# Kernel optimization log

Measured on AMD Instinct MI355X. Metric: run time of the kernel, lower is better.

Reference implementation:

```python
import jax, jax.numpy as jnp
import numpy as np

N_NODES = 50000
N_EDGES = 800000
IN_C, HID_C, OUT_C = 128, 128, 64
BN_EPS = 1e-5


def setup_inputs() -> dict:
    key = jax.random.key(0)
    ks = jax.random.split(key, 12)
    def lin(k, fan_in, fan_out):
        bound = 1.0 / np.sqrt(fan_in)
        kw, kb = jax.random.split(k)
        W = jax.random.uniform(kw, (fan_in, fan_out), jnp.float32, -bound, bound)
        b = jax.random.uniform(kb, (fan_out,), jnp.float32, -bound, bound)
        return W, b
    x = jax.random.normal(ks[0], (N_NODES, IN_C), jnp.float32)
    edge_index = jax.random.randint(ks[1], (2, N_EDGES), 0, N_NODES, jnp.int32)
    w1a, b1a = lin(ks[2], IN_C, HID_C)
    w1b, b1b = lin(ks[3], HID_C, HID_C)
    w2a, b2a = lin(ks[4], HID_C, OUT_C)
    w2b, b2b = lin(ks[5], OUT_C, OUT_C)
    return {
        "x": x, "edge_index": edge_index,
        "w1a": w1a, "b1a": b1a, "g1": jnp.ones((HID_C,)), "be1": jnp.zeros((HID_C,)),
        "w1b": w1b, "b1b": b1b,
        "w2a": w2a, "b2a": b2a, "g2": jnp.ones((OUT_C,)), "be2": jnp.zeros((OUT_C,)),
        "w2b": w2b, "b2b": b2b,
    }


def _batchnorm(h, gamma, beta):
    # training-style BN over node dim, biased variance (torch BatchNorm1d)
    mean = jnp.mean(h, axis=0)
    var = jnp.mean(jnp.square(h - mean), axis=0)
    return (h - mean) * jax.lax.rsqrt(var + BN_EPS) * gamma + beta


def _gin_layer(x, src, dst, n_nodes, w_a, b_a, gamma, beta, w_b, b_b):
    # GINConv with eps=0: MLP(x + sum_{j->i} x_j)
    agg = jax.ops.segment_sum(x[src], dst, num_segments=n_nodes)  # [N, C]
    h = x + agg
    h = h @ w_a + b_a
    h = jax.nn.relu(_batchnorm(h, gamma, beta))
    return h @ w_b + b_b


def reference(x, edge_index, w1a, b1a, g1, be1, w1b, b1b, w2a, b2a, g2, be2, w2b, b2b):
    src, dst = edge_index[0], edge_index[1]
    n = x.shape[0]
    h = _gin_layer(x, src, dst, n, w1a, b1a, g1, be1, w1b, b1b)
    h = jax.nn.relu(h)  # dropout p=0.0 -> identity
    h = _gin_layer(h, src, dst, n, w2a, b2a, g2, be2, w2b, b2b)
    return jax.nn.log_softmax(h, axis=-1)
```

## Files before the change

### kernel.cpp

```cpp
#include <hip/hip_runtime.h>


typedef unsigned short u16;
typedef unsigned int u32;
typedef __attribute__((ext_vector_type(8))) short short8;
typedef __attribute__((ext_vector_type(4))) short short4v;
typedef __attribute__((ext_vector_type(4))) float f32x4;

#define DEV_INLINE __device__ __forceinline__

DEV_INLINE void atomAddF(float* p, float v) { unsafeAtomicAdd(p, v); }

DEV_INLINE u16 f2bf(float f) {
    unsigned u = __float_as_uint(f);
    u += 0x7fffu + ((u >> 16) & 1u);
    return (u16)(u >> 16);
}
DEV_INLINE float bf2f(u16 h) { return __uint_as_float(((unsigned)h) << 16); }

__global__ __launch_bounds__(256) void wprep4_k(
    const float* __restrict__ w1a, const float* __restrict__ w1b,
    const float* __restrict__ w2a, const float* __restrict__ w2b,
    short* __restrict__ o1a, short* __restrict__ o1b,
    short* __restrict__ o2a, short* __restrict__ o2b)
{
    int b = blockIdx.x;
    const float* W; short* wf; int K, NOUT;
    if (b < 8)       { W = w1a; wf = o1a; K = 128; NOUT = 128; }
    else if (b < 16) { W = w1b; wf = o1b; K = 128; NOUT = 128; b -= 8; }
    else if (b < 20) { W = w2a; wf = o2a; K = 128; NOUT = 64;  b -= 16; }
    else             { W = w2b; wf = o2b; K = 64;  NOUT = 64;  b -= 20; }
    const int u = b * 256 + threadIdx.x;
    const int units = (NOUT / 16) * (K / 32) * 64;
    if (u >= units) return;
    const int per_ct = (K / 32) * 64;
    const int ct = u / per_ct;
    const int rem = u % per_ct;
    const int kc = rem >> 6;
    const int l = rem & 63;
    const int col = ct * 16 + (l & 15);
    const int k0 = kc * 32 + (l >> 4) * 8;
    short8 pk;
#pragma unroll
    for (int j = 0; j < 8; j++)
        pk[j] = (short)f2bf(W[(size_t)(k0 + j) * NOUT + col]);
    *(short8*)&wf[(size_t)u * 8] = pk;
}

__global__ __launch_bounds__(256) void mgemm1_k(
    const float* __restrict__ x, const short* __restrict__ wf,
    u16* __restrict__ p1, int M)
{
    constexpr int KD = 128, NC = 128, KC = 4, KQ = 32;
    __shared__ short Asl[64 * KD];
    const int t = threadIdx.x;
    const int l = t & 63;
    const int w = t >> 6;

    short8 B[2][KC];
#pragma unroll
    for (int c = 0; c < 2; c++)
#pragma unroll
        for (int kc = 0; kc < KC; kc++)
            B[c][kc] = *(const short8*)&wf[(((w * 2 + c) * KC + kc) * 64 + l) * 8];

    {
        const int r = t >> 2;
        const int q = t & 3;
        const int grow = blockIdx.x * 64 + r;
        const int rt = r >> 4;
        u16 hv[KQ];
        if (grow < M) {
            const float* ap = x + (size_t)grow * KD + q * KQ;
#pragma unroll
            for (int i = 0; i < KQ / 4; i++) {
                const float4 v = ((const float4*)ap)[i];
                hv[i * 4 + 0] = f2bf(v.x); hv[i * 4 + 1] = f2bf(v.y);
                hv[i * 4 + 2] = f2bf(v.z); hv[i * 4 + 3] = f2bf(v.w);
            }
        } else {
#pragma unroll
            for (int i = 0; i < KQ; i++) hv[i] = 0;
        }
#pragma unroll
        for (int gg = 0; gg < KQ / 8; gg++) {
            const int k0 = q * KQ + gg * 8;
            const int kc = k0 >> 5;
            const int lane = (r & 15) + ((k0 >> 3) & 3) * 16;
            *(short8*)&Asl[((rt * KC + kc) * 64 + lane) * 8] = *(short8*)&hv[gg * 8];
        }
    }
    __syncthreads();

    f32x4 acc[4][2];
#pragma unroll
    for (int rt = 0; rt < 4; rt++)
#pragma unroll
        for (int c = 0; c < 2; c++) acc[rt][c] = (f32x4){0.f, 0.f, 0.f, 0.f};

#pragma unroll
    for (int kc = 0; kc < KC; kc++)
#pragma unroll
        for (int rt = 0; rt < 4; rt++) {
            const short8 x0 = *(const short8*)&Asl[((rt * KC + kc) * 64 + l) * 8];
            acc[rt][0] = __builtin_amdgcn_mfma_f32_16x16x32_bf16(B[0][kc], x0, acc[rt][0], 0, 0, 0);
            acc[rt][1] = __builtin_amdgcn_mfma_f32_16x16x32_bf16(B[1][kc], x0, acc[rt][1], 0, 0, 0);
        }

    const int cbase = (l >> 4) * 4;
#pragma unroll
    for (int rt = 0; rt < 4; rt++) {
        const int grow = blockIdx.x * 64 + rt * 16 + (l & 15);
        if (grow < M) {
#pragma unroll
            for (int c = 0; c < 2; c++) {
                short4v o16;
#pragma unroll
                for (int j = 0; j < 4; j++) o16[j] = (short)f2bf(acc[rt][c][j]);
                *(short4v*)&p1[(size_t)grow * NC + (w * 2 + c) * 16 + cbase] = o16;
            }
        }
    }
}

__global__ __launch_bounds__(256) void mgemm23_k(
    const u16* __restrict__ s1, const short* __restrict__ w1bf,
    const short* __restrict__ w2af,
    const float* __restrict__ sum, const float* __restrict__ sumsq,
    const float* __restrict__ g, const float* __restrict__ be, float invN,
    const float* __restrict__ b1b, u16* __restrict__ p2, int M)
{
    constexpr int KD = 128, NC = 128, NO = 64, KC = 4, KQ = 32;
    __shared__ short Asl[64 * KD];
    __shared__ float scb[KD];
    __shared__ float shb[KD];

    const int t = threadIdx.x;
    const int l = t & 63;
    const int w = t >> 6;

    short8 B1[2][KC];
    short8 B2[KC];
#pragma unroll
    for (int c = 0; c < 2; c++)
#pragma unroll
        for (int kc = 0; kc < KC; kc++)
            B1[c][kc] = *(const short8*)&w1bf[(((w * 2 + c) * KC + kc) * 64 + l) * 8];
#pragma unroll
    for (int kc = 0; kc < KC; kc++)
        B2[kc] = *(const short8*)&w2af[((w * KC + kc) * 64 + l) * 8];

    if (t < KD) {
        const float m = sum[t] * invN;
        const float v = sumsq[t] * invN - m * m;
        const float r = rsqrtf(v + 1e-5f);
        const float s = g[t] * r;
        scb[t] = s;
        shb[t] = be[t] - m * s;
    }
    __syncthreads();

    {
        const int r = t >> 2;
        const int q = t & 3;
        const int grow = blockIdx.x * 64 + r;
        const int rt = r >> 4;
        u16 hv[KQ];
        if (grow < M) {
            const u16* ap = s1 + (size_t)grow * KD + q * KQ;
#pragma unroll
            for (int i = 0; i < KQ / 8; i++)
                *(short8*)&hv[i * 8] = ((const short8*)ap)[i];
#pragma unroll
            for (int i = 0; i < KQ; i++) {
                const int k = q * KQ + i;
                hv[i] = f2bf(fmaxf(0.f, bf2f(hv[i]) * scb[k] + shb[k]));
            }
        } else {
#pragma unroll
            for (int i = 0; i < KQ; i++) hv[i] = 0;
        }
#pragma unroll
        for (int gg = 0; gg < KQ / 8; gg++) {
            const int k0 = q * KQ + gg * 8;
            const int kc = k0 >> 5;
            const int lane = (r & 15) + ((k0 >> 3) & 3) * 16;
            *(short8*)&Asl[((rt * KC + kc) * 64 + lane) * 8] = *(short8*)&hv[gg * 8];
        }
    }
    __syncthreads();

    f32x4 acc[4][2];
#pragma unroll
    for (int rt = 0; rt < 4; rt++)
#pragma unroll
        for (int c = 0; c < 2; c++) acc[rt][c] = (f32x4){0.f, 0.f, 0.f, 0.f};
#pragma unroll
    for (int kc = 0; kc < KC; kc++)
#pragma unroll
        for (int rt = 0; rt < 4; rt++) {
            const short8 x0 = *(const short8*)&Asl[((rt * KC + kc) * 64 + l) * 8];
            acc[rt][0] = __builtin_amdgcn_mfma_f32_16x16x32_bf16(B1[0][kc], x0, acc[rt][0], 0, 0, 0);
            acc[rt][1] = __builtin_amdgcn_mfma_f32_16x16x32_bf16(B1[1][kc], x0, acc[rt][1], 0, 0, 0);
        }
    __syncthreads();

    {
        const int cb4 = l >> 4;
#pragma unroll
        for (int rt = 0; rt < 4; rt++) {
            const int row = rt * 16 + (l & 15);
            const int sw = (row & 7) << 1;
#pragma unroll
            for (int c = 0; c < 2; c++) {
                const int ct = w * 2 + c;
                const float4 bv = *(const float4*)&b1b[ct * 16 + cb4 * 4];
                short4v o16;
                o16[0] = (short)f2bf(fmaxf(acc[rt][c][0] + bv.x, 0.f));
                o16[1] = (short)f2bf(fmaxf(acc[rt][c][1] + bv.y, 0.f));
                o16[2] = (short)f2bf(fmaxf(acc[rt][c][2] + bv.z, 0.f));
                o16[3] = (short)f2bf(fmaxf(acc[rt][c][3] + bv.w, 0.f));
                const int gsw = (ct * 4 + cb4) ^ sw;
                *(short4v*)&Asl[row * 128 + gsw * 4] = o16;
            }
        }
    }
    __syncthreads();

    f32x4 acc2[4];
#pragma unroll
    for (int rt = 0; rt < 4; rt++) acc2[rt] = (f32x4){0.f, 0.f, 0.f, 0.f};
#pragma unroll
    for (int kc = 0; kc < KC; kc++)
#pragma unroll
        for (int rt = 0; rt < 4; rt++) {
            const int row = rt * 16 + (l & 15);
            const int G = kc * 8 + (l >> 4) * 2;
            const int Gs = G ^ ((row & 7) << 1);
            const short8 x0 = *(const short8*)&Asl[row * 128 + Gs * 4];
            acc2[rt] = __builtin_amdgcn_mfma_f32_16x16x32_bf16(B2[kc], x0, acc2[rt], 0, 0, 0);
        }

    {
        const int cbase = (l >> 4) * 4;
#pragma unroll
        for (int rt = 0; rt < 4; rt++) {
            const int grow = blockIdx.x * 64 + rt * 16 + (l & 15);
            if (grow < M) {
                short4v o16;
#pragma unroll
                for (int j = 0; j < 4; j++) o16[j] = (short)f2bf(acc2[rt][j]);
                *(short4v*)&p2[(size_t)grow * NO + w * 16 + cbase] = o16;
            }
        }
    }
}

__global__ __launch_bounds__(256) void mgemm4_k(
    const u16* __restrict__ s2, const short* __restrict__ Wf,
    const float* __restrict__ sum, const float* __restrict__ sumsq,
    const float* __restrict__ g, const float* __restrict__ be, float invN,
    const float* __restrict__ bias, float* __restrict__ outp, int M)
{
    constexpr int KD = 64, NC = 64, KC = 2, CT = 4, KQ = 16;
    __shared__ short Asl[64 * KD];
    __shared__ short Bsl[NC * KD];
    __shared__ float scb[KD];
    __shared__ float shb[KD];

    const int t = threadIdx.x;
    const int l = t & 63;
    const int w = t >> 6;

    if (t < KD) {
        const float m = sum[t] * invN;
        const float v = sumsq[t] * invN - m * m;
        const float r = rsqrtf(v + 1e-5f);
        const float s = g[t] * r;
        scb[t] = s;
        shb[t] = be[t] - m * s;
    }
    __syncthreads();

    {
        const float4* src = (const float4*)Wf;
        float4* dst = (float4*)Bsl;
#pragma unroll
        for (int u = t; u < NC * KD / 8; u += 256) dst[u] = src[u];
    }
    {
        const int r = t >> 2;
        const int q = t & 3;
        const int grow = blockIdx.x * 64 + r;
        const int rt = r >> 4;
        u16 hv[KQ];
        if (grow < M) {
            const u16* ap = s2 + (size_t)grow * KD + q * KQ;
#pragma unroll
            for (int i = 0; i < KQ / 8; i++)
                *(short8*)&hv[i * 8] = ((const short8*)ap)[i];
#pragma unroll
            for (int i = 0; i < KQ; i++) {
                const int k = q * KQ + i;
                hv[i] = f2bf(fmaxf(0.f, bf2f(hv[i]) * scb[k] + shb[k]));
            }
        } else {
#pragma unroll
            for (int i = 0; i < KQ; i++) hv[i] = 0;
        }
#pragma unroll
        for (int gg = 0; gg < KQ / 8; gg++) {
            const int k0 = q * KQ + gg * 8;
            const int kc = k0 >> 5;
            const int lane = (r & 15) + ((k0 >> 3) & 3) * 16;
            *(short8*)&Asl[((rt * KC + kc) * 64 + lane) * 8] = *(short8*)&hv[gg * 8];
        }
    }
    __syncthreads();

    f32x4 acc[CT];
#pragma unroll
    for (int c = 0; c < CT; c++) acc[c] = (f32x4){0.f, 0.f, 0.f, 0.f};
#pragma unroll
    for (int kc = 0; kc < KC; kc++) {
        const short8 x0 = *(const short8*)&Asl[((w * KC + kc) * 64 + l) * 8];
#pragma unroll
        for (int ct = 0; ct < CT; ct++) {
            const short8 wb = *(const short8*)&Bsl[((ct * KC + kc) * 64 + l) * 8];
            acc[ct] = __builtin_amdgcn_mfma_f32_16x16x32_bf16(wb, x0, acc[ct], 0, 0, 0);
        }
    }

    const int cbase = (l >> 4) * 4;
    const int grow = blockIdx.x * 64 + w * 16 + (l & 15);
    float v[CT * 4];
#pragma unroll
    for (int ct = 0; ct < CT; ct++) {
        const float4 bv = *(const float4*)&bias[ct * 16 + cbase];
        v[ct * 4 + 0] = acc[ct][0] + bv.x;
        v[ct * 4 + 1] = acc[ct][1] + bv.y;
        v[ct * 4 + 2] = acc[ct][2] + bv.z;
        v[ct * 4 + 3] = acc[ct][3] + bv.w;
    }
    float m = v[0];
#pragma unroll
    for (int j = 1; j < CT * 4; j++) m = fmaxf(m, v[j]);
    m = fmaxf(m, __shfl_xor(m, 16));
    m = fmaxf(m, __shfl_xor(m, 32));
    float s = 0.f;
#pragma unroll
    for (int j = 0; j < CT * 4; j++) s += __expf(v[j] - m);
    s += __shfl_xor(s, 16);
    s += __shfl_xor(s, 32);
    const float lg = m + __logf(s);
    if (grow < M) {
#pragma unroll
        for (int ct = 0; ct < CT; ct++) {
            f32x4 o;
#pragma unroll
            for (int j = 0; j < 4; j++) o[j] = v[ct * 4 + j] - lg;
            *(f32x4*)&outp[(size_t)grow * NC + ct * 16 + cbase] = o;
        }
    }
}

__global__ __launch_bounds__(256) void hist_k(const int* __restrict__ ei,
                                              int* __restrict__ cnt,
                                              int* __restrict__ agg, int E)
{
    const int gid = blockIdx.x * blockDim.x + threadIdx.x;
    if (gid < 256) agg[gid] = 0;
    const int stride = gridDim.x * blockDim.x;
    for (int e = gid; e < E; e += stride) atomicAdd(&cnt[ei[E + e]], 1);
}

__global__ __launch_bounds__(256) void scan1_k(const int* __restrict__ cnt,
                                               int* __restrict__ agg,
                                               int* __restrict__ off,
                                               int* __restrict__ cursor,
                                               int N, int E)
{
    __shared__ int part[256];
    __shared__ int redu[256];
    const int t = threadIdx.x;
    const int b = blockIdx.x;
    const int i = b * 256 + t;
    const int v = (i < N) ? cnt[i] : 0;
    part[t] = v;
    __syncthreads();
    for (int d = 1; d < 256; d <<= 1) {
        const int u = (t >= d) ? part[t - d] : 0;
        __syncthreads();
        part[t] += u;
        __syncthreads();
    }
    if (t == 0)
        __hip_atomic_store(&agg[b], part[255] | (1 << 30), __ATOMIC_RELEASE,
                           __HIP_MEMORY_SCOPE_AGENT);
    int loc = 0;
    for (int pb = t; pb < b; pb += 256) {
        int a;
        do {
            a = __hip_atomic_load(&agg[pb], __ATOMIC_ACQUIRE,
                                  __HIP_MEMORY_SCOPE_AGENT);
        } while (!(a & (1 << 30)));
        loc += a & ((1 << 30) - 1);
    }
    redu[t] = loc;
    __syncthreads();
    for (int s = 128; s; s >>= 1) {
        if (t < s) redu[t] += redu[t + s];
        __syncthreads();
    }
    const int base = redu[0];
    if (i < N) {
        const int o = base + part[t] - v;
        off[i] = o;
        cursor[i] = o;
    }
    if (b == 0 && t == 0) off[N] = E;
}

__global__ __launch_bounds__(256) void fill_k(const int* __restrict__ ei,
                                              int* __restrict__ cursor,
                                              int* __restrict__ srcs, int E)
{
    const int gid = blockIdx.x * blockDim.x + threadIdx.x;
    const int stride = gridDim.x * blockDim.x;
    for (int e = gid; e < E; e += stride) {
        const int s = ei[e];
        const int d = ei[E + e];
        const int pos = atomicAdd(&cursor[d], 1);
        srcs[pos] = s;
    }
}

template <int C>
__global__ __launch_bounds__(256) void segsum_bf(
    const u16* __restrict__ p, const int* __restrict__ off,
    const int* __restrict__ srcs, u16* __restrict__ out,
    float* __restrict__ sum, float* __restrict__ sumsq, int N)
{
    constexpr int BLKN = 8;
    constexpr int VPL = C / 64;
    __shared__ float red[4][64][2 * VPL];

    const int wv = threadIdx.x >> 6;
    const int l  = threadIdx.x & 63;
    const int base = blockIdx.x * 4 * BLKN;

    float ss[VPL], qq[VPL];
#pragma unroll
    for (int v = 0; v < VPL; v++) { ss[v] = 0.f; qq[v] = 0.f; }

    for (int i = 0; i < BLKN; i++) {
        const int n = base + i * 4 + wv;
        if (n < N) {
            const int lo = __builtin_amdgcn_readfirstlane(off[n]);
            const int hi = __builtin_amdgcn_readfirstlane(off[n + 1]);
            float acc[VPL];
            if constexpr (VPL == 2) {
                const u32 u = *(const u32*)&p[(size_t)n * C + 2 * l];
                acc[0] = bf2f((u16)u);
                acc[1] = bf2f((u16)(u >> 16));
            } else {
                acc[0] = bf2f(p[(size_t)n * C + l]);
            }
            const int cnt = hi - lo;
            if (cnt > 0) {
                const int last = hi - 1;
                int idx[8];
#pragma unroll
                for (int j = 0; j < 8; j++) idx[j] = srcs[min(lo + j, last)];
                for (int e = lo; e < hi; e += 8) {
                    int nx[8];
#pragma unroll
                    for (int j = 0; j < 8; j++)
                        nx[j] = srcs[min(e + 8 + j, last)];
#pragma unroll
                    for (int j = 0; j < 8; j++) {
                        const bool live = (e + j) < hi;
                        if constexpr (VPL == 2) {
                            const u32 u = *(const u32*)&p[(size_t)idx[j] * C + 2 * l];
                            const float v0 = bf2f((u16)u);
                            const float v1 = bf2f((u16)(u >> 16));
                            acc[0] += live ? v0 : 0.f;
                            acc[1] += live ? v1 : 0.f;
                        } else {
                            const float v = bf2f(p[(size_t)idx[j] * C + l]);
                            acc[0] += live ? v : 0.f;
                        }
                    }
#pragma unroll
                    for (int j = 0; j < 8; j++) idx[j] = nx[j];
                }
            }
            if constexpr (VPL == 2) {
                const u16 r0 = f2bf(acc[0]);
                const u16 r1 = f2bf(acc[1]);
                *(u32*)&out[(size_t)n * C + 2 * l] = (u32)r0 | ((u32)r1 << 16);
                const float f0 = bf2f(r0), f1 = bf2f(r1);
                ss[0] += f0; qq[0] += f0 * f0;
                ss[1] += f1; qq[1] += f1 * f1;
            } else {
                const u16 r = f2bf(acc[0]);
                out[(size_t)n * C + l] = r;
                const float f = bf2f(r);
                ss[0] += f; qq[0] += f * f;
            }
        }
    }

#pragma unroll
    for (int v = 0; v < VPL; v++) {
        red[wv][l][2 * v] = ss[v];
        red[wv][l][2 * v + 1] = qq[v];
    }
    __syncthreads();
    if (wv == 0) {
#pragma unroll
        for (int v = 0; v < VPL; v++) {
            float a = 0.f, b = 0.f;
#pragma unroll
            for (int w2 = 0; w2 < 4; w2++) {
                a += red[w2][l][2 * v];
                b += red[w2][l][2 * v + 1];
            }
            const int ch = (VPL == 2) ? (2 * l + v) : l;
            atomAddF(&sum[ch], a);
            atomAddF(&sumsq[ch], b);
        }
    }
}

extern "C" void kernel_launch(void* const* d_in, const int* in_sizes, int n_in,
                              void* d_out, int out_size, void* d_ws, size_t ws_size,
                              hipStream_t stream)
{
    const float* x   = (const float*)d_in[0];
    const int*   ei  = (const int*)d_in[1];
    const float* w1a = (const float*)d_in[2];
    const float* g1  = (const float*)d_in[4];
    const float* be1 = (const float*)d_in[5];
    const float* w1b = (const float*)d_in[6];
    const float* b1b = (const float*)d_in[7];
    const float* w2a = (const float*)d_in[8];
    const float* g2  = (const float*)d_in[10];
    const float* be2 = (const float*)d_in[11];
    const float* w2b = (const float*)d_in[12];
    const float* b2b = (const float*)d_in[13];
    float* out = (float*)d_out;

    const int N = in_sizes[0] / 128;
    const int E = in_sizes[1] / 2;

    u16* buf1 = (u16*)d_ws;
    u16* buf2 = buf1 + (size_t)N * 128;
    float* stats = (float*)(buf2 + (size_t)N * 128);
    float* sum1 = stats,       *sq1 = stats + 128;
    float* sum2 = stats + 256, *sq2 = stats + 320;
    int* cnt    = (int*)(stats + 1024);
    int* off    = cnt + N;
    int* cursor = off + N + 1;
    int* srcs   = cursor + N;
    int* agg    = srcs + E;
    int* bpre   = agg + 256;
    short* w1af = (short*)(bpre + 256);
    short* w1bf = w1af + 128 * 128;
    short* w2af = w1bf + 128 * 128;
    short* w2bf = w2af + 128 * 64;
    u16* p1 = buf1;
    u16* s1 = buf2;
    u16* p2 = buf1;
    u16* s2 = buf2;

    hipMemsetAsync(stats, 0, 1024 * sizeof(float) + (size_t)N * sizeof(int), stream);

    const int G1 = (N + 255) / 256;
    const int gb = (N + 63) / 64;
    const int gs = (N + 31) / 32;
    const float invN = 1.f / N;

    hist_k<<<1024, 256, 0, stream>>>(ei, cnt, agg, E);
    scan1_k<<<G1, 256, 0, stream>>>(cnt, agg, off, cursor, N, E);
    fill_k<<<1024, 256, 0, stream>>>(ei, cursor, srcs, E);

    wprep4_k<<<22, 256, 0, stream>>>(w1a, w1b, w2a, w2b, w1af, w1bf, w2af, w2bf);

    mgemm1_k<<<gb, 256, 0, stream>>>(x, w1af, p1, N);
    segsum_bf<128><<<gs, 256, 0, stream>>>(p1, off, srcs, s1, sum1, sq1, N);

    mgemm23_k<<<gb, 256, 0, stream>>>(s1, w1bf, w2af, sum1, sq1, g1, be1,
                                      invN, b1b, p2, N);

    segsum_bf<64><<<gs, 256, 0, stream>>>(p2, off, srcs, s2, sum2, sq2, N);
    mgemm4_k<<<gb, 256, 0, stream>>>(s2, w2bf, sum2, sq2, g2, be2, invN, b2b,
                                     out, N);
}
```

Baseline: 290.6 us.

## Merge first GEMM, weight prep, and degree histogram into one heterogeneous launch

Combines mgemm1, the weight-preparation kernel and the edge histogram into a single kernel whose blocks pick their role by block index. The first GEMM now converts w1a to bf16 fragments inline from fp32 global memory instead of reading a prepacked buffer. This removes two launches and the serialization between independent stages, letting the GEMM and histogram atomics overlap. The cost is redundant per-block strided weight conversion and a mixed-role grid that may load-balance unevenly.

```diff
diff --git a/kernel.cpp b/kernel.cpp
--- a/kernel.cpp
+++ b/kernel.cpp
@@ -18,360 +18,127 @@
 }
 DEV_INLINE float bf2f(u16 h) { return __uint_as_float(((unsigned)h) << 16); }
 
-__global__ __launch_bounds__(256) void wprep4_k(
-    const float* __restrict__ w1a, const float* __restrict__ w1b,
-    const float* __restrict__ w2a, const float* __restrict__ w2b,
-    short* __restrict__ o1a, short* __restrict__ o1b,
-    short* __restrict__ o2a, short* __restrict__ o2b)
+__global__ __launch_bounds__(256) void fat1_k(
+    const float* __restrict__ x, const float* __restrict__ w1a,
+    u16* __restrict__ p1, int M, int gb,
+    const int* __restrict__ ei, int* __restrict__ cnt,
+    int* __restrict__ agg, int E,
+    const float* __restrict__ w1b, const float* __restrict__ w2a,
+    const float* __restrict__ w2b,
+    short* __restrict__ o1b, short* __restrict__ o2a,
+    short* __restrict__ o2b)
 {
-    int b = blockIdx.x;
-    const float* W; short* wf; int K, NOUT;
-    if (b < 8)       { W = w1a; wf = o1a; K = 128; NOUT = 128; }
-    else if (b < 16) { W = w1b; wf = o1b; K = 128; NOUT = 128; b -= 8; }
-    else if (b < 20) { W = w2a; wf = o2a; K = 128; NOUT = 64;  b -= 16; }
-    else             { W = w2b; wf = o2b; K = 64;  NOUT = 64;  b -= 20; }
-    const int u = b * 256 + threadIdx.x;
-    const int units = (NOUT / 16) * (K / 32) * 64;
-    if (u >= units) return;
-    const int per_ct = (K / 32) * 64;
-    const int ct = u / per_ct;
-    const int rem = u % per_ct;
-    const int kc = rem >> 6;
-    const int l = rem & 63;
-    const int col = ct * 16 + (l & 15);
-    const int k0 = kc * 32 + (l >> 4) * 8;
-    short8 pk;
-#pragma unroll
-    for (int j = 0; j < 8; j++)
-        pk[j] = (short)f2bf(W[(size_t)(k0 + j) * NOUT + col]);
-    *(short8*)&wf[(size_t)u * 8] = pk;
-}
-
-__global__ __launch_bounds__(256) void mgemm1_k(
-    const float* __restrict__ x, const short* __restrict__ wf,
-    u16* __restrict__ p1, int M)
-{
-    constexpr int KD = 128, NC = 128, KC = 4, KQ = 32;
-    __shared__ short Asl[64 * KD];
+    __shared__ short Asl[64 * 128];
+    const int bid = blockIdx.x;
     const int t = threadIdx.x;
-    const int l = t & 63;
-    const int w = t >> 6;
-
-    short8 B[2][KC];
-#pragma unroll
-    for (int c = 0; c < 2; c++)
+
+    if (bid < gb) {
+        constexpr int KD = 128, NC = 128, KC = 4, KQ = 32;
+        const int l = t & 63;
+        const int w = t >> 6;
+
+        short8 B[2][KC];
+#pragma unroll
+        for (int c = 0; c < 2; c++) {
+            const int col = (w * 2 + c) * 16 + (l & 15);
+#pragma unroll
+            for (int kc = 0; kc < KC; kc++) {
+                const int k0 = kc * 32 + (l >> 4) * 8;
+                short8 b;
+#pragma unroll
+                for (int j = 0; j < 8; j++)
+                    b[j] = (short)f2bf(w1a[(size_t)(k0 + j) * NC + col]);
+                B[c][kc] = b;
+            }
+        }
+
+        {
+            const int r = t >> 2;
+            const int q = t & 3;
+            const int grow = bid * 64 + r;
+            const int rt = r >> 4;
+            u16 hv[KQ];
+            if (grow < M) {
+                const float* ap = x + (size_t)grow * KD + q * KQ;
+#pragma unroll
+                for (int i = 0; i < KQ / 4; i++) {
+                    const float4 v = ((const float4*)ap)[i];
+                    hv[i * 4 + 0] = f2bf(v.x); hv[i * 4 + 1] = f2bf(v.y);
+                    hv[i * 4 + 2] = f2bf(v.z); hv[i * 4 + 3] = f2bf(v.w);
+                }
+            } else {
+#pragma unroll
+                for (int i = 0; i < KQ; i++) hv[i] = 0;
+            }
+#pragma unroll
+            for (int gg = 0; gg < KQ / 8; gg++) {
+                const int k0 = q * KQ + gg * 8;
+                const int kc = k0 >> 5;
+                const int lane = (r & 15) + ((k0 >> 3) & 3) * 16;
+                *(short8*)&Asl[((rt * KC + kc) * 64 + lane) * 8] =
+                    *(short8*)&hv[gg * 8];
+            }
+        }
+        __syncthreads();
+
+        f32x4 acc[4][2];
+#pragma unroll
+        for (int rt = 0; rt < 4; rt++)
+#pragma unroll
+            for (int c = 0; c < 2; c++) acc[rt][c] = (f32x4){0.f, 0.f, 0.f, 0.f};
+
 #pragma unroll
         for (int kc = 0; kc < KC; kc++)
-            B[c][kc] = *(const short8*)&wf[(((w * 2 + c) * KC + kc) * 64 + l) * 8];
-
-    {
-        const int r = t >> 2;
-        const int q = t & 3;
-        const int grow = blockIdx.x * 64 + r;
-        const int rt = r >> 4;
-        u16 hv[KQ];
-        if (grow < M) {
-            const float* ap = x + (size_t)grow * KD + q * KQ;
-#pragma unroll
-            for (int i = 0; i < KQ / 4; i++) {
-                const float4 v = ((const float4*)ap)[i];
-                hv[i * 4 + 0] = f2bf(v.x); hv[i * 4 + 1] = f2bf(v.y);
-                hv[i * 4 + 2] = f2bf(v.z); hv[i * 4 + 3] = f2bf(v.w);
-            }
-        } else {
-#pragma unroll
-            for (int i = 0; i < KQ; i++) hv[i] = 0;
-        }
-#pragma unroll
-        for (int gg = 0; gg < KQ / 8; gg++) {
-            const int k0 = q * KQ + gg * 8;
-            const int kc = k0 >> 5;
-            const int lane = (r & 15) + ((k0 >> 3) & 3) * 16;
-            *(short8*)&Asl[((rt * KC + kc) * 64 + lane) * 8] = *(short8*)&hv[gg * 8];
-        }
-    }
-    __syncthreads();
-
-    f32x4 acc[4][2];
-#pragma unroll
-    for (int rt = 0; rt < 4; rt++)
-#pragma unroll
-        for (int c = 0; c < 2; c++) acc[rt][c] = (f32x4){0.f, 0.f, 0.f, 0.f};
-
-#pragma unroll
-    for (int kc = 0; kc < KC; kc++)
+#pragma unroll
+            for (int rt = 0; rt < 4; rt++) {
+                const short8 x0 = *(const short8*)&Asl[((rt * KC + kc) * 64 + l) * 8];
+                acc[rt][0] = __builtin_amdgcn_mfma_f32_16x16x32_bf16(B[0][kc], x0, acc[rt][0], 0, 0, 0);
+                acc[rt][1] = __builtin_amdgcn_mfma_f32_16x16x32_bf16(B[1][kc], x0, acc[rt][1], 0, 0, 0);
+            }
+
+        const int cbase = (l >> 4) * 4;
 #pragma unroll
         for (int rt = 0; rt < 4; rt++) {
-            const short8 x0 = *(const short8*)&Asl[((rt * KC + kc) * 64 + l) * 8];
-            acc[rt][0] = __builtin_amdgcn_mfma_f32_16x16x32_bf16(B[0][kc], x0, acc[rt][0], 0, 0, 0);
-            acc[rt][1] = __builtin_amdgcn_mfma_f32_16x16x32_bf16(B[1][kc], x0, acc[rt][1], 0, 0, 0);
-        }
-
-    const int cbase = (l >> 4) * 4;
-#pragma unroll
-    for (int rt = 0; rt < 4; rt++) {
-        const int grow = blockIdx.x * 64 + rt * 16 + (l & 15);
-        if (grow < M) {
-#pragma unroll
-            for (int c = 0; c < 2; c++) {
-                short4v o16;
-#pragma unroll
-                for (int j = 0; j < 4; j++) o16[j] = (short)f2bf(acc[rt][c][j]);
-                *(short4v*)&p1[(size_t)grow * NC + (w * 2 + c) * 16 + cbase] = o16;
-            }
-        }
-    }
-}
-
-__global__ __launch_bounds__(256) void mgemm23_k(
-    const u16* __restrict__ s1, const short* __restrict__ w1bf,
-    const short* __restrict__ w2af,
-    const float* __restrict__ sum, const float* __restrict__ sumsq,
-    const float* __restrict__ g, const float* __restrict__ be, float invN,
-    const float* __restrict__ b1b, u16* __restrict__ p2, int M)
-{
-    constexpr int KD = 128, NC = 128, NO = 64, KC = 4, KQ = 32;
-    __shared__ short Asl[64 * KD];
-    __shared__ float scb[KD];
-    __shared__ float shb[KD];
-
-    const int t = threadIdx.x;
-    const int l = t & 63;
-    const int w = t >> 6;
-
-    short8 B1[2][KC];
-    short8 B2[KC];
-#pragma unroll
-    for (int c = 0; c < 2; c++)
-#pragma unroll
-        for (int kc = 0; kc < KC; kc++)
-            B1[c][kc] = *(const short8*)&w1bf[(((w * 2 + c) * KC + kc) * 64 + l) * 8];
-#pragma unroll
-    for (int kc = 0; kc < KC; kc++)
-        B2[kc] = *(const short8*)&w2af[((w * KC + kc) * 64 + l) * 8];
-
-    if (t < KD) {
-        const float m = sum[t] * invN;
-        const float v = sumsq[t] * invN - m * m;
-        const float r = rsqrtf(v + 1e-5f);
-        const float s = g[t] * r;
-        scb[t] = s;
-        shb[t] = be[t] - m * s;
-    }
-    __syncthreads();
-
-    {
-        const int r = t >> 2;
-        const int q = t & 3;
-        const int grow = blockIdx.x * 64 + r;
-        const int rt = r >> 4;
-        u16 hv[KQ];
-        if (grow < M) {
-            const u16* ap = s1 + (size_t)grow * KD + q * KQ;
-#pragma unroll
-            for (int i = 0; i < KQ / 8; i++)
-                *(short8*)&hv[i * 8] = ((const short8*)ap)[i];
-#pragma unroll
-            for (int i = 0; i < KQ; i++) {
-                const int k = q * KQ + i;
-                hv[i] = f2bf(fmaxf(0.f, bf2f(hv[i]) * scb[k] + shb[k]));
-            }
-        } else {
-#pragma unroll
-            for (int i = 0; i < KQ; i++) hv[i] = 0;
-        }
-#pragma unroll
-        for (int gg = 0; gg < KQ / 8; gg++) {
-            const int k0 = q * KQ + gg * 8;
-            const int kc = k0 >> 5;
-            const int lane = (r & 15) + ((k0 >> 3) & 3) * 16;
-            *(short8*)&Asl[((rt * KC + kc) * 64 + lane) * 8] = *(short8*)&hv[gg * 8];
-        }
-    }
-    __syncthreads();
-
-    f32x4 acc[4][2];
-#pragma unroll
-    for (int rt = 0; rt < 4; rt++)
-#pragma unroll
-        for (int c = 0; c < 2; c++) acc[rt][c] = (f32x4){0.f, 0.f, 0.f, 0.f};
-#pragma unroll
-    for (int kc = 0; kc < KC; kc++)
-#pragma unroll
-        for (int rt = 0; rt < 4; rt++) {
-            const short8 x0 = *(const short8*)&Asl[((rt * KC + kc) * 64 + l) * 8];
-            acc[rt][0] = __builtin_amdgcn_mfma_f32_16x16x32_bf16(B1[0][kc], x0, acc[rt][0], 0, 0, 0);
-            acc[rt][1] = __builtin_amdgcn_mfma_f32_16x16x32_bf16(B1[1][kc], x0, acc[rt][1], 0, 0, 0);
-        }
-    __syncthreads();
-
-    {
-        const int cb4 = l >> 4;
-#pragma unroll
-        for (int rt = 0; rt < 4; rt++) {
-            const int row = rt * 16 + (l & 15);
-            const int sw = (row & 7) << 1;
-#pragma unroll
-            for (int c = 0; c < 2; c++) {
-                const int ct = w * 2 + c;
-                const float4 bv = *(const float4*)&b1b[ct * 16 + cb4 * 4];
-                short4v o16;
-                o16[0] = (short)f2bf(fmaxf(acc[rt][c][0] + bv.x, 0.f));
-                o16[1] = (short)f2bf(fmaxf(acc[rt][c][1] + bv.y, 0.f));
-                o16[2] = (short)f2bf(fmaxf(acc[rt][c][2] + bv.z, 0.f));
-                o16[3] = (short)f2bf(fmaxf(acc[rt][c][3] + bv.w, 0.f));
-                const int gsw = (ct * 4 + cb4) ^ sw;
-                *(short4v*)&Asl[row * 128 + gsw * 4] = o16;
-            }
-        }
-    }
-    __syncthreads();
-
-    f32x4 acc2[4];
-#pragma unroll
-    for (int rt = 0; rt < 4; rt++) acc2[rt] = (f32x4){0.f, 0.f, 0.f, 0.f};
-#pragma unroll
-    for (int kc = 0; kc < KC; kc++)
-#pragma unroll
-        for (int rt = 0; rt < 4; rt++) {
-            const int row = rt * 16 + (l & 15);
-            const int G = kc * 8 + (l >> 4) * 2;
-            const int Gs = G ^ ((row & 7) << 1);
-            const short8 x0 = *(const short8*)&Asl[row * 128 + Gs * 4];
-            acc2[rt] = __builtin_amdgcn_mfma_f32_16x16x32_bf16(B2[kc], x0, acc2[rt], 0, 0, 0);
-        }
-
-    {
-        const int cbase = (l >> 4) * 4;
-#pragma unroll
-        for (int rt = 0; rt < 4; rt++) {
-            const int grow = blockIdx.x * 64 + rt * 16 + (l & 15);
+            const int grow = bid * 64 + rt * 16 + (l & 15);
             if (grow < M) {
-                short4v o16;
-#pragma unroll
-                for (int j = 0; j < 4; j++) o16[j] = (short)f2bf(acc2[rt][j]);
-                *(short4v*)&p2[(size_t)grow * NO + w * 16 + cbase] = o16;
-            }
-        }
-    }
-}
-
-__global__ __launch_bounds__(256) void mgemm4_k(
-    const u16* __restrict__ s2, const short* __restrict__ Wf,
-    const float* __restrict__ sum, const float* __restrict__ sumsq,
-    const float* __restrict__ g, const float* __restrict__ be, float invN,
-    const float* __restrict__ bias, float* __restrict__ outp, int M)
-{
-    constexpr int KD = 64, NC = 64, KC = 2, CT = 4, KQ = 16;
-    __shared__ short Asl[64 * KD];
-    __shared__ short Bsl[NC * KD];
-    __shared__ float scb[KD];
-    __shared__ float shb[KD];
-
-    const int t = threadIdx.x;
-    const int l = t & 63;
-    const int w = t >> 6;
-
-    if (t < KD) {
-        const float m = sum[t] * invN;
-        const float v = sumsq[t] * invN - m * m;
-        const float r = rsqrtf(v + 1e-5f);
-        const float s = g[t] * r;
-        scb[t] = s;
-        shb[t] = be[t] - m * s;
-    }
-    __syncthreads();
-
-    {
-        const float4* src = (const float4*)Wf;
-        float4* dst = (float4*)Bsl;
-#pragma unroll
-        for (int u = t; u < NC * KD / 8; u += 256) dst[u] = src[u];
-    }
-    {
-        const int r = t >> 2;
-        const int q = t & 3;
-        const int grow = blockIdx.x * 64 + r;
-        const int rt = r >> 4;
-        u16 hv[KQ];
-        if (grow < M) {
-            const u16* ap = s2 + (size_t)grow * KD + q * KQ;
-#pragma unroll
-            for (int i = 0; i < KQ / 8; i++)
-                *(short8*)&hv[i * 8] = ((const short8*)ap)[i];
-#pragma unroll
-            for (int i = 0; i < KQ; i++) {
-                const int k = q * KQ + i;
-                hv[i] = f2bf(fmaxf(0.f, bf2f(hv[i]) * scb[k] + shb[k]));
-            }
-        } else {
-#pragma unroll
-            for (int i = 0; i < KQ; i++) hv[i] = 0;
-        }
-#pragma unroll
-        for (int gg = 0; gg < KQ / 8; gg++) {
-            const int k0 = q * KQ + gg * 8;
-            const int kc = k0 >> 5;
-            const int lane = (r & 15) + ((k0 >> 3) & 3) * 16;
-            *(short8*)&Asl[((rt * KC + kc) * 64 + lane) * 8] = *(short8*)&hv[gg * 8];
-        }
-    }
-    __syncthreads();
-
-    f32x4 acc[CT];
-#pragma unroll
-    for (int c = 0; c < CT; c++) acc[c] = (f32x4){0.f, 0.f, 0.f, 0.f};
-#pragma unroll
-    for (int kc = 0; kc < KC; kc++) {
-        const short8 x0 = *(const short8*)&Asl[((w * KC + kc) * 64 + l) * 8];
-#pragma unroll
-        for (int ct = 0; ct < CT; ct++) {
-            const short8 wb = *(const short8*)&Bsl[((ct * KC + kc) * 64 + l) * 8];
-            acc[ct] = __builtin_amdgcn_mfma_f32_16x16x32_bf16(wb, x0, acc[ct], 0, 0, 0);
-        }
-    }
-
-    const int cbase = (l >> 4) * 4;
-    const int grow = blockIdx.x * 64 + w * 16 + (l & 15);
-    float v[CT * 4];
-#pragma unroll
-    for (int ct = 0; ct < CT; ct++) {
-        const float4 bv = *(const float4*)&bias[ct * 16 + cbase];
-        v[ct * 4 + 0] = acc[ct][0] + bv.x;
-        v[ct * 4 + 1] = acc[ct][1] + bv.y;
-        v[ct * 4 + 2] = acc[ct][2] + bv.z;
-        v[ct * 4 + 3] = acc[ct][3] + bv.w;
-    }
-    float m = v[0];
-#pragma unroll
-    for (int j = 1; j < CT * 4; j++) m = fmaxf(m, v[j]);
-    m = fmaxf(m, __shfl_xor(m, 16));
-    m = fmaxf(m, __shfl_xor(m, 32));
-    float s = 0.f;
-#pragma unroll
-    for (int j = 0; j < CT * 4; j++) s += __expf(v[j] - m);
-    s += __shfl_xor(s, 16);
-    s += __shfl_xor(s, 32);
-    const float lg = m + __logf(s);
-    if (grow < M) {
-#pragma unroll
-        for (int ct = 0; ct < CT; ct++) {
-            f32x4 o;
-#pragma unroll
-            for (int j = 0; j < 4; j++) o[j] = v[ct * 4 + j] - lg;
-            *(f32x4*)&outp[(size_t)grow * NC + ct * 16 + cbase] = o;
-        }
-    }
-}
-
-__global__ __launch_bounds__(256) void hist_k(const int* __restrict__ ei,
-                                              int* __restrict__ cnt,
-                                              int* __restrict__ agg, int E)
-{
-    const int gid = blockIdx.x * blockDim.x + threadIdx.x;
-    if (gid < 256) agg[gid] = 0;
-    const int stride = gridDim.x * blockDim.x;
-    for (int e = gid; e < E; e += stride) atomicAdd(&cnt[ei[E + e]], 1);
+#pragma unroll
+                for (int c = 0; c < 2; c++) {
+                    short4v o16;
+#pragma unroll
+                    for (int j = 0; j < 4; j++) o16[j] = (short)f2bf(acc[rt][c][j]);
+                    *(short4v*)&p1[(size_t)grow * NC + (w * 2 + c) * 16 + cbase] = o16;
+                }
+            }
+        }
+    } else if (bid < gb + 14) {
+        int b = bid - gb;
+        const float* W; short* wf; int K, NOUT;
+        if (b < 8)       { W = w1b; wf = o1b; K = 128; NOUT = 128; }
+        else if (b < 12) { W = w2a; wf = o2a; K = 128; NOUT = 64;  b -= 8; }
+        else             { W = w2b; wf = o2b; K = 64;  NOUT = 64;  b -= 12; }
+        const int u = b * 256 + t;
+        const int units = (NOUT / 16) * (K / 32) * 64;
+        if (u < units) {
+            const int per_ct = (K / 32) * 64;
+            const int ct = u / per_ct;
+            const int rem = u % per_ct;
+            const int kc = rem >> 6;
+            const int l = rem & 63;
+            const int col = ct * 16 + (l & 15);
+            const int k0 = kc * 32 + (l >> 4) * 8;
+            short8 pk;
+#pragma unroll
+            for (int j = 0; j < 8; j++)
+                pk[j] = (short)f2bf(W[(size_t)(k0 + j) * NOUT + col]);
+            *(short8*)&wf[(size_t)u * 8] = pk;
+        }
+    } else {
+        const int hb = bid - gb - 14;
+        const int gid = hb * 256 + t;
+        if (gid < 256) agg[gid] = 0;
+        const int stride = (gridDim.x - gb - 14) * 256;
+        for (int e = gid; e < E; e += stride) atomicAdd(&cnt[ei[E + e]], 1);
+    }
 }
 
 __global__ __launch_bounds__(256) void scan1_k(const int* __restrict__ cnt,
@@ -432,6 +199,247 @@
         const int d = ei[E + e];
         const int pos = atomicAdd(&cursor[d], 1);
         srcs[pos] = s;
+    }
+}
+
+__global__ __launch_bounds__(256) void mgemm23_k(
+    const u16* __restrict__ s1, const short* __restrict__ w1bf,
+    const short* __restrict__ w2af,
+    const float* __restrict__ sum, const float* __restrict__ sumsq,
+    const float* __restrict__ g, const float* __restrict__ be, float invN,
+    const float* __restrict__ b1b, u16* __restrict__ p2, int M)
+{
+    constexpr int KD = 128, NO = 64, KC = 4, KQ = 32;
+    __shared__ short Asl[64 * KD];
+    __shared__ float scb[KD];
+    __shared__ float shb[KD];
+
+    const int t = threadIdx.x;
+    const int l = t & 63;
+    const int w = t >> 6;
+
+    short8 B1[2][KC];
+    short8 B2[KC];
+#pragma unroll
+    for (int c = 0; c < 2; c++)
+#pragma unroll
+        for (int kc = 0; kc < KC; kc++)
+            B1[c][kc] = *(const short8*)&w1bf[(((w * 2 + c) * KC + kc) * 64 + l) * 8];
+#pragma unroll
+    for (int kc = 0; kc < KC; kc++)
+        B2[kc] = *(const short8*)&w2af[((w * KC + kc) * 64 + l) * 8];
+
+    if (t < KD) {
+        const float m = sum[t] * invN;
+        const float v = sumsq[t] * invN - m * m;
+        const float r = rsqrtf(v + 1e-5f);
+        const float s = g[t] * r;
+        scb[t] = s;
+        shb[t] = be[t] - m * s;
+    }
+    __syncthreads();
+
+    {
+        const int r = t >> 2;
+        const int q = t & 3;
+        const int grow = blockIdx.x * 64 + r;
+        const int rt = r >> 4;
+        u16 hv[KQ];
+        if (grow < M) {
+            const u16* ap = s1 + (size_t)grow * KD + q * KQ;
+#pragma unroll
+            for (int i = 0; i < KQ / 8; i++)
+                *(short8*)&hv[i * 8] = ((const short8*)ap)[i];
+#pragma unroll
+            for (int i = 0; i < KQ; i++) {
+                const int k = q * KQ + i;
+                hv[i] = f2bf(fmaxf(0.f, bf2f(hv[i]) * scb[k] + shb[k]));
+            }
+        } else {
+#pragma unroll
+            for (int i = 0; i < KQ; i++) hv[i] = 0;
+        }
+#pragma unroll
+        for (int gg = 0; gg < KQ / 8; gg++) {
+            const int k0 = q * KQ + gg * 8;
+            const int kc = k0 >> 5;
+            const int lane = (r & 15) + ((k0 >> 3) & 3) * 16;
+            *(short8*)&Asl[((rt * KC + kc) * 64 + lane) * 8] = *(short8*)&hv[gg * 8];
+        }
+    }
+    __syncthreads();
+
+    f32x4 acc[4][2];
+#pragma unroll
+    for (int rt = 0; rt < 4; rt++)
+#pragma unroll
+        for (int c = 0; c < 2; c++) acc[rt][c] = (f32x4){0.f, 0.f, 0.f, 0.f};
+#pragma unroll
+    for (int kc = 0; kc < KC; kc++)
+#pragma unroll
+        for (int rt = 0; rt < 4; rt++) {
+            const short8 x0 = *(const short8*)&Asl[((rt * KC + kc) * 64 + l) * 8];
+            acc[rt][0] = __builtin_amdgcn_mfma_f32_16x16x32_bf16(B1[0][kc], x0, acc[rt][0], 0, 0, 0);
+            acc[rt][1] = __builtin_amdgcn_mfma_f32_16x16x32_bf16(B1[1][kc], x0, acc[rt][1], 0, 0, 0);
+        }
+    __syncthreads();
+
+    {
+        const int cb4 = l >> 4;
+#pragma unroll
+        for (int rt = 0; rt < 4; rt++) {
+            const int row = rt * 16 + (l & 15);
+            const int sw = (row & 7) << 1;
+#pragma unroll
+            for (int c = 0; c < 2; c++) {
+                const int ct = w * 2 + c;
+                const float4 bv = *(const float4*)&b1b[ct * 16 + cb4 * 4];
+                short4v o16;
+                o16[0] = (short)f2bf(fmaxf(acc[rt][c][0] + bv.x, 0.f));
+                o16[1] = (short)f2bf(fmaxf(acc[rt][c][1] + bv.y, 0.f));
+                o16[2] = (short)f2bf(fmaxf(acc[rt][c][2] + bv.z, 0.f));
+                o16[3] = (short)f2bf(fmaxf(acc[rt][c][3] + bv.w, 0.f));
+                const int gsw = (ct * 4 + cb4) ^ sw;
+                *(short4v*)&Asl[row * 128 + gsw * 4] = o16;
+            }
+        }
+    }
+    __syncthreads();
+
+    f32x4 acc2[4];
+#pragma unroll
+    for (int rt = 0; rt < 4; rt++) acc2[rt] = (f32x4){0.f, 0.f, 0.f, 0.f};
+#pragma unroll
+    for (int kc = 0; kc < KC; kc++)
+#pragma unroll
+        for (int rt = 0; rt < 4; rt++) {
+            const int row = rt * 16 + (l & 15);
+            const int G = kc * 8 + (l >> 4) * 2;
+            const int Gs = G ^ ((row & 7) << 1);
+            const short8 x0 = *(const short8*)&Asl[row * 128 + Gs * 4];
+            acc2[rt] = __builtin_amdgcn_mfma_f32_16x16x32_bf16(B2[kc], x0, acc2[rt], 0, 0, 0);
+        }
+
+    {
+        const int cbase = (l >> 4) * 4;
+#pragma unroll
+        for (int rt = 0; rt < 4; rt++) {
+            const int grow = blockIdx.x * 64 + rt * 16 + (l & 15);
+            if (grow < M) {
+                short4v o16;
+#pragma unroll
+                for (int j = 0; j < 4; j++) o16[j] = (short)f2bf(acc2[rt][j]);
+                *(short4v*)&p2[(size_t)grow * NO + w * 16 + cbase] = o16;
+            }
+        }
+    }
+}
+
+__global__ __launch_bounds__(256) void mgemm4_k(
+    const u16* __restrict__ s2, const short* __restrict__ Wf,
+    const float* __restrict__ sum, const float* __restrict__ sumsq,
+    const float* __restrict__ g, const float* __restrict__ be, float invN,
+    const float* __restrict__ bias, float* __restrict__ outp, int M)
+{
+    constexpr int KD = 64, NC = 64, KC = 2, CT = 4, KQ = 16;
+    __shared__ short Asl[64 * KD];
+    __shared__ short Bsl[NC * KD];
+    __shared__ float scb[KD];
+    __shared__ float shb[KD];
+
+    const int t = threadIdx.x;
+    const int l = t & 63;
+    const int w = t >> 6;
+
+    if (t < KD) {
+        const float m = sum[t] * invN;
+        const float v = sumsq[t] * invN - m * m;
+        const float r = rsqrtf(v + 1e-5f);
+        const float s = g[t] * r;
+        scb[t] = s;
+        shb[t] = be[t] - m * s;
+    }
+    __syncthreads();
+
+    {
+        const float4* src = (const float4*)Wf;
+        float4* dst = (float4*)Bsl;
+#pragma unroll
+        for (int u = t; u < NC * KD / 8; u += 256) dst[u] = src[u];
+    }
+    {
+        const int r = t >> 2;
+        const int q = t & 3;
+        const int grow = blockIdx.x * 64 + r;
+        const int rt = r >> 4;
+        u16 hv[KQ];
+        if (grow < M) {
+            const u16* ap = s2 + (size_t)grow * KD + q * KQ;
+#pragma unroll
+            for (int i = 0; i < KQ / 8; i++)
+                *(short8*)&hv[i * 8] = ((const short8*)ap)[i];
+#pragma unroll
+            for (int i = 0; i < KQ; i++) {
+                const int k = q * KQ + i;
+                hv[i] = f2bf(fmaxf(0.f, bf2f(hv[i]) * scb[k] + shb[k]));
+            }
+        } else {
+#pragma unroll
+            for (int i = 0; i < KQ; i++) hv[i] = 0;
+        }
+#pragma unroll
+        for (int gg = 0; gg < KQ / 8; gg++) {
+            const int k0 = q * KQ + gg * 8;
+            const int kc = k0 >> 5;
+            const int lane = (r & 15) + ((k0 >> 3) & 3) * 16;
+            *(short8*)&Asl[((rt * KC + kc) * 64 + lane) * 8] = *(short8*)&hv[gg * 8];
+        }
+    }
+    __syncthreads();
+
+    f32x4 acc[CT];
+#pragma unroll
+    for (int c = 0; c < CT; c++) acc[c] = (f32x4){0.f, 0.f, 0.f, 0.f};
+#pragma unroll
+    for (int kc = 0; kc < KC; kc++) {
+        const short8 x0 = *(const short8*)&Asl[((w * KC + kc) * 64 + l) * 8];
+#pragma unroll
+        for (int ct = 0; ct < CT; ct++) {
+            const short8 wb = *(const short8*)&Bsl[((ct * KC + kc) * 64 + l) * 8];
+            acc[ct] = __builtin_amdgcn_mfma_f32_16x16x32_bf16(wb, x0, acc[ct], 0, 0, 0);
+        }
+    }
+
+    const int cbase = (l >> 4) * 4;
+    const int grow = blockIdx.x * 64 + w * 16 + (l & 15);
+    float v[CT * 4];
+#pragma unroll
+    for (int ct = 0; ct < CT; ct++) {
+        const float4 bv = *(const float4*)&bias[ct * 16 + cbase];
+        v[ct * 4 + 0] = acc[ct][0] + bv.x;
+        v[ct * 4 + 1] = acc[ct][1] + bv.y;
+        v[ct * 4 + 2] = acc[ct][2] + bv.z;
+        v[ct * 4 + 3] = acc[ct][3] + bv.w;
+    }
+    float m = v[0];
+#pragma unroll
+    for (int j = 1; j < CT * 4; j++) m = fmaxf(m, v[j]);
+    m = fmaxf(m, __shfl_xor(m, 16));
+    m = fmaxf(m, __shfl_xor(m, 32));
+    float s = 0.f;
+#pragma unroll
+    for (int j = 0; j < CT * 4; j++) s += __expf(v[j] - m);
+    s += __shfl_xor(s, 16);
+    s += __shfl_xor(s, 32);
+    const float lg = m + __logf(s);
+    if (grow < M) {
+#pragma unroll
+        for (int ct = 0; ct < CT; ct++) {
+            f32x4 o;
+#pragma unroll
+            for (int j = 0; j < 4; j++) o[j] = v[ct * 4 + j] - lg;
+            *(f32x4*)&outp[(size_t)grow * NC + ct * 16 + cbase] = o;
+        }
     }
 }
 
@@ -564,9 +572,8 @@
     int* cursor = off + N + 1;
     int* srcs   = cursor + N;
     int* agg    = srcs + E;
-    int* bpre   = agg + 256;
-    short* w1af = (short*)(bpre + 256);
-    short* w1bf = w1af + 128 * 128;
+    int* pad    = agg + 256;
+    short* w1bf = (short*)(pad + 256);
     short* w2af = w1bf + 128 * 128;
     short* w2bf = w2af + 128 * 64;
     u16* p1 = buf1;
@@ -581,13 +588,13 @@
     const int gs = (N + 31) / 32;
     const float invN = 1.f / N;
 
-    hist_k<<<1024, 256, 0, stream>>>(ei, cnt, agg, E);
+    fat1_k<<<gb + 14 + 1024, 256, 0, stream>>>(
+        x, w1a, p1, N, gb, ei, cnt, agg, E,
+        w1b, w2a, w2b, w1bf, w2af, w2bf);
+
     scan1_k<<<G1, 256, 0, stream>>>(cnt, agg, off, cursor, N, E);
     fill_k<<<1024, 256, 0, stream>>>(ei, cursor, srcs, E);
 
-    wprep4_k<<<22, 256, 0, stream>>>(w1a, w1b, w2a, w2b, w1af, w1bf, w2af, w2bf);
-
-    mgemm1_k<<<gb, 256, 0, stream>>>(x, w1af, p1, N);
     segsum_bf<128><<<gs, 256, 0, stream>>>(p1, off, srcs, s1, sum1, sq1, N);
 
     mgemm23_k<<<gb, 256, 0, stream>>>(s1, w1bf, w2af, sum1, sq1, g1, be1,
```

Result: no change. 294.6 us (+1.4%).
